# Performance work log

Hardware: AMD Instinct MI355X
Metric: run time of the kernel (lower is better)

The kernel has to match this reference:

```python
import jax, jax.numpy as jnp
import numpy as np

B = 16384          # batch (parallel envs)
D_OBS = 512        # num_actor_obs
A = 32             # num_actions
E = 8              # num_experts
K = 2              # top_k
GH = [256, 128]    # gating hidden dims
EH = [1024, 512, 256]  # expert hidden dims


def _linear_init(key, fan_in, fan_out, extra=()):
    kw, kb = jax.random.split(key)
    scale = 1.0 / np.sqrt(fan_in)
    w = jax.random.uniform(kw, extra + (fan_in, fan_out), jnp.float32, -scale, scale)
    b = jax.random.uniform(kb, extra + (fan_out,), jnp.float32, -scale, scale)
    return w, b


def setup_inputs() -> dict:
    key = jax.random.key(0)
    ks = jax.random.split(key, 8)
    obs = jax.random.normal(ks[0], (B, D_OBS), jnp.float32)
    # gating network: D_OBS -> 256 -> 128 -> E
    gw1, gb1 = _linear_init(ks[1], D_OBS, GH[0])
    gw2, gb2 = _linear_init(ks[2], GH[0], GH[1])
    gw3, gb3 = _linear_init(ks[3], GH[1], E)
    # experts (stacked over expert axis): D_OBS -> 1024 -> 512 -> 256 -> A
    ew1, eb1 = _linear_init(ks[4], D_OBS, EH[0], (E,))
    ew2, eb2 = _linear_init(ks[5], EH[0], EH[1], (E,))
    ew3, eb3 = _linear_init(ks[6], EH[1], EH[2], (E,))
    ew4, eb4 = _linear_init(ks[7], EH[2], A, (E,))
    return {
        "observations": obs,
        "gw1": gw1, "gb1": gb1, "gw2": gw2, "gb2": gb2, "gw3": gw3, "gb3": gb3,
        "ew1": ew1, "eb1": eb1, "ew2": ew2, "eb2": eb2,
        "ew3": ew3, "eb3": eb3, "ew4": ew4, "eb4": eb4,
    }


def reference(observations, gw1, gb1, gw2, gb2, gw3, gb3,
              ew1, eb1, ew2, eb2, ew3, eb3, ew4, eb4):
    elu = jax.nn.elu
    # --- gating network ---
    g = elu(observations @ gw1 + gb1)
    g = elu(g @ gw2 + gb2)
    gate_logits = g @ gw3 + gb3                      # [B, E]
    gate_probs = jax.nn.softmax(gate_logits, axis=-1)
    # --- top-k selection and renormalization ---
    topk_w, topk_idx = jax.lax.top_k(gate_probs, K)  # [B, K]
    topk_w = topk_w / jnp.sum(topk_w, axis=-1, keepdims=True)
    # --- run all experts as batched GEMMs (same math as masked dispatch) ---
    h = elu(jnp.einsum('bi,eio->beo', observations, ew1) + eb1)  # [B, E, 1024]
    h = elu(jnp.einsum('beo,eoh->beh', h, ew2) + eb2)            # [B, E, 512]
    h = elu(jnp.einsum('beh,ehf->bef', h, ew3) + eb3)            # [B, E, 256]
    expert_out = jnp.einsum('bef,efa->bea', h, ew4) + eb4        # [B, E, A]
    # --- weighted combine over selected experts ---
    onehot = jax.nn.one_hot(topk_idx, E, dtype=topk_w.dtype)     # [B, K, E]
    combine_w = jnp.einsum('bk,bke->be', topk_w, onehot)         # [B, E]
    action_mean = jnp.einsum('be,bea->ba', combine_w, expert_out)  # [B, A]
    return action_mean
```

## Files before the change

### kernel.cpp

```cpp
#include <hip/hip_runtime.h>
#include <hip/hip_bf16.h>

typedef __bf16 v8bf __attribute__((ext_vector_type(8)));
typedef float  v4f  __attribute__((ext_vector_type(4)));

#define B_ROWS 16384
#define NSLOTS 32768
#define MAXTILES 264

#define OFF_W1T   0u
#define OFF_W2T   8388608u
#define OFF_W3T   16777216u
#define OFF_W4T   18874368u
#define OFF_META  19005440u
#define OFF_SEL   19009536u
#define OFF_W01   19075072u
#define OFF_ROWL  19206144u
#define OFF_WL    19337216u
#define OFF_Q     19468288u
#define OFF_G1    OFF_Q
#define OFF_G2    (OFF_Q + 16777216u)
#define OFF_X1    OFF_Q
#define OFF_H2    OFF_Q
#define OFF_EO    OFF_Q
#define OFF_H1    (OFF_Q + 33554432u)
#define OFF_H3    OFF_H1
#define WS_NEED   (OFF_H1 + 67108864u)


__device__ __forceinline__ void gload_lds16(const void* g, void* l) {
  __builtin_amdgcn_global_load_lds(
      (const __attribute__((address_space(1))) void*)g,
      (__attribute__((address_space(3))) void*)l, 16, 0, 0);
}

__device__ __forceinline__ float elu_f(float x) {
  return x > 0.f ? x : expm1f(x);
}

__global__ __launch_bounds__(256) void transpose_convert(
    const float* __restrict__ in, __hip_bfloat16* __restrict__ outp, int R, int C) {
  __shared__ __align__(16) float tile[32][33];
  int e = blockIdx.z;
  const float* src = in + (size_t)e * R * C;
  __hip_bfloat16* dst = outp + (size_t)e * R * C;
  int r0 = blockIdx.x * 32, c0 = blockIdx.y * 32;
  int tr = threadIdx.x >> 5, tc = threadIdx.x & 31;
#pragma unroll
  for (int q = 0; q < 4; ++q)
    tile[tr + 8*q][tc] = src[(size_t)(r0 + tr + 8*q) * C + c0 + tc];
  __syncthreads();
#pragma unroll
  for (int q = 0; q < 4; ++q)
    dst[(size_t)(c0 + tr + 8*q) * R + r0 + tc] = __float2bfloat16(tile[tc][tr + 8*q]);
}

__global__ __launch_bounds__(256) void sgemm_elu(
    const float* __restrict__ A, const float* __restrict__ Bm,
    const float* __restrict__ bias, float* __restrict__ C,
    int M, int N, int K) {
  __shared__ __align__(16) float sA[16][132];
  __shared__ __align__(16) float sB[16][68];
  int tid = threadIdx.x;
  int tx = tid & 15, ty = tid >> 4;
  int m0 = blockIdx.x * 128, n0 = blockIdx.y * 64;
  float acc[8][4] = {};
  for (int k0 = 0; k0 < K; k0 += 16) {
    {
      int m = tid >> 1, ks = (tid & 1) * 8;
      const float* ap = &A[(size_t)(m0 + m) * K + k0 + ks];
      float4 v0 = *(const float4*)ap;
      float4 v1 = *(const float4*)(ap + 4);
      sA[ks+0][m] = v0.x; sA[ks+1][m] = v0.y; sA[ks+2][m] = v0.z; sA[ks+3][m] = v0.w;
      sA[ks+4][m] = v1.x; sA[ks+5][m] = v1.y; sA[ks+6][m] = v1.z; sA[ks+7][m] = v1.w;
    }
    {
      int kr = tid >> 4, nn = (tid & 15) * 4;
      *(float4*)&sB[kr][nn] = *(const float4*)&Bm[(size_t)(k0 + kr) * N + n0 + nn];
    }
    __syncthreads();
#pragma unroll
    for (int kk = 0; kk < 16; ++kk) {
      float a[8], b[4];
      *(float4*)&a[0] = *(const float4*)&sA[kk][ty*8];
      *(float4*)&a[4] = *(const float4*)&sA[kk][ty*8+4];
      *(float4*)&b[0] = *(const float4*)&sB[kk][tx*4];
#pragma unroll
      for (int i = 0; i < 8; ++i)
#pragma unroll
        for (int j = 0; j < 4; ++j)
          acc[i][j] = fmaf(a[i], b[j], acc[i][j]);
    }
    __syncthreads();
  }
  float bs[4];
#pragma unroll
  for (int j = 0; j < 4; ++j) bs[j] = bias[n0 + tx*4 + j];
#pragma unroll
  for (int i = 0; i < 8; ++i) {
    int m = m0 + ty*8 + i;
    float4 o;
    o.x = elu_f(acc[i][0] + bs[0]);
    o.y = elu_f(acc[i][1] + bs[1]);
    o.z = elu_f(acc[i][2] + bs[2]);
    o.w = elu_f(acc[i][3] + bs[3]);
    *(float4*)&C[(size_t)m * N + n0 + tx*4] = o;
  }
}

__global__ __launch_bounds__(256) void gate3_topk(
    const float* __restrict__ G2, const float* __restrict__ gw3,
    const float* __restrict__ gb3, int* __restrict__ sel01,
    float2* __restrict__ w01, int* __restrict__ meta) {
  __shared__ __align__(16) float g2t[64][132];
  __shared__ __align__(16) float w3[1024];
  __shared__ float b3[8];
  __shared__ int lc[8];
  int tid = threadIdx.x;
  int row0 = blockIdx.x * 64;
  {
    int r = tid >> 5, f = (tid & 31) * 4;
#pragma unroll
    for (int rr = 0; rr < 64; rr += 8)
      *(float4*)&g2t[r + rr][f] = *(const float4*)&G2[(size_t)(row0 + r + rr) * 128 + f];
  }
  ((float4*)w3)[tid] = ((const float4*)gw3)[tid];
  if (tid < 8) { b3[tid] = gb3[tid]; lc[tid] = 0; }
  __syncthreads();
  if (tid < 64) {
    int row = row0 + tid;
    float lg[8];
#pragma unroll
    for (int e = 0; e < 8; ++e) lg[e] = b3[e];
    for (int k = 0; k < 128; ++k) {
      float x = g2t[tid][k];
#pragma unroll
      for (int e = 0; e < 8; ++e) lg[e] = fmaf(x, w3[k*8 + e], lg[e]);
    }
    float mx = lg[0];
#pragma unroll
    for (int e = 1; e < 8; ++e) mx = fmaxf(mx, lg[e]);
    float p[8], s = 0.f;
#pragma unroll
    for (int e = 0; e < 8; ++e) { p[e] = expf(lg[e] - mx); s += p[e]; }
    float inv = 1.f / s;
#pragma unroll
    for (int e = 0; e < 8; ++e) p[e] *= inv;
    int i0 = 0; float v0 = p[0];
#pragma unroll
    for (int e = 1; e < 8; ++e) if (p[e] > v0) { v0 = p[e]; i0 = e; }
    int i1 = -1; float v1 = -1.f;
#pragma unroll
    for (int e = 0; e < 8; ++e) if (e != i0 && p[e] > v1) { v1 = p[e]; i1 = e; }
    float sw = 1.f / (v0 + v1);
    sel01[row] = i0 | (i1 << 8);
    w01[row] = make_float2(v0 * sw, v1 * sw);
    atomicAdd(&lc[i0], 1);
    atomicAdd(&lc[i1], 1);
  }
  __syncthreads();
  if (tid < 8) atomicAdd(&meta[1 + tid], lc[tid]);
}

__global__ void build_tiles(int* __restrict__ meta) {
  if (threadIdx.x != 0) return;
  int base = 0, nt = 0;
  for (int e = 0; e < 8; ++e) {
    int c = meta[1 + e];
    meta[17 + e] = base;
    for (int j = 0; j < c; j += 128) {
      meta[32 + nt]  = e;
      meta[296 + nt] = base + j;
      meta[560 + nt] = (c - j < 128) ? (c - j) : 128;
      nt++;
    }
    base += c;
  }
  meta[0] = nt;
}

__global__ __launch_bounds__(256) void scatter_rows(
    const int* __restrict__ sel01, float2* __restrict__ w01,
    int* __restrict__ meta, int* __restrict__ rowlist, float* __restrict__ wlist) {
  __shared__ int lc[8];
  __shared__ int gb[8];
  int tid = threadIdx.x;
  if (tid < 8) lc[tid] = 0;
  __syncthreads();
  int row = blockIdx.x * 256 + tid;
  int s = sel01[row];
  int e0 = s & 255, e1 = (s >> 8) & 255;
  float2 w = w01[row];
  int l0 = atomicAdd(&lc[e0], 1);
  int l1 = atomicAdd(&lc[e1], 1);
  __syncthreads();
  if (tid < 8) gb[tid] = atomicAdd(&meta[9 + tid], lc[tid]);
  __syncthreads();
  int s0 = meta[17 + e0] + gb[e0] + l0;
  int s1 = meta[17 + e1] + gb[e1] + l1;
  rowlist[s0] = row; wlist[s0] = w.x;
  rowlist[s1] = row; wlist[s1] = w.y;
  ((int2*)w01)[row] = make_int2(s0, s1);
}

__global__ __launch_bounds__(256) void gather_convert(
    const float* __restrict__ obs, const int* __restrict__ rowlist,
    __hip_bfloat16* __restrict__ X1) {
  int tid = threadIdx.x;
  int slot = blockIdx.x * 4 + (tid >> 6);
  int l = tid & 63;
  int row = rowlist[slot];
  const float* src = obs + (size_t)row * 512 + l * 8;
  float4 a = *(const float4*)src;
  float4 b = *(const float4*)(src + 4);
  union { __hip_bfloat16 h[8]; uint4 u; } t;
  t.h[0] = __float2bfloat16(a.x); t.h[1] = __float2bfloat16(a.y);
  t.h[2] = __float2bfloat16(a.z); t.h[3] = __float2bfloat16(a.w);
  t.h[4] = __float2bfloat16(b.x); t.h[5] = __float2bfloat16(b.y);
  t.h[6] = __float2bfloat16(b.z); t.h[7] = __float2bfloat16(b.w);
  *(uint4*)(X1 + (size_t)slot * 512 + l * 8) = t.u;
}

__global__ __launch_bounds__(256) void moe_gemm(
    const __hip_bfloat16* __restrict__ A, const __hip_bfloat16* __restrict__ BT,
    const float* __restrict__ bias, __hip_bfloat16* __restrict__ C,
    const int* __restrict__ meta, int N, int K) {
  int t = blockIdx.x;
  if (t >= meta[0]) return;
  int e    = meta[32 + t];
  int m0   = meta[296 + t];
  int rows = meta[560 + t];
  int n0   = blockIdx.y * 128;

  __shared__ __align__(16) __hip_bfloat16 sA[128 * 32];
  __shared__ __align__(16) __hip_bfloat16 sB[128 * 32];

  int tid = threadIdx.x;
  int w = tid >> 6, l = tid & 63;
  int lr = l >> 2;
  int lk = (l & 3) * 8;
  int wm = w >> 1, wn = w & 1;
  int ml = l & 15, kq = l >> 4;

  const __hip_bfloat16* BTe = BT + (size_t)e * N * K;
  v4f acc[4][4] = {};

  for (int k0 = 0; k0 < K; k0 += 32) {
#pragma unroll
    for (int it = 0; it < 2; ++it) {
      int r = it * 64 + w * 16 + lr;
      int gr = m0 + (r < rows ? r : rows - 1);
      gload_lds16(A + (size_t)gr * K + k0 + lk, &sA[(it * 64 + w * 16) * 32]);
    }
#pragma unroll
    for (int it = 0; it < 2; ++it) {
      int r = it * 64 + w * 16 + lr;
      gload_lds16(BTe + (size_t)(n0 + r) * K + k0 + lk, &sB[(it * 64 + w * 16) * 32]);
    }
    __syncthreads();
    v8bf af[4], bf[4];
#pragma unroll
    for (int i = 0; i < 4; ++i)
      af[i] = *(const v8bf*)&sA[(wm * 64 + i * 16 + ml) * 32 + kq * 8];
#pragma unroll
    for (int j = 0; j < 4; ++j)
      bf[j] = *(const v8bf*)&sB[(wn * 64 + j * 16 + ml) * 32 + kq * 8];
#pragma unroll
    for (int i = 0; i < 4; ++i)
#pragma unroll
      for (int j = 0; j < 4; ++j)
        acc[i][j] = __builtin_amdgcn_mfma_f32_16x16x32_bf16(af[i], bf[j], acc[i][j], 0, 0, 0);
    __syncthreads();
  }

  int rl0 = kq * 4;
#pragma unroll
  for (int j = 0; j < 4; ++j) {
    int col = n0 + wn * 64 + j * 16 + ml;
    float bs = bias[(size_t)e * N + col];
#pragma unroll
    for (int i = 0; i < 4; ++i) {
#pragma unroll
      for (int r = 0; r < 4; ++r) {
        int rl = wm * 64 + i * 16 + rl0 + r;
        if (rl < rows) {
          float v = elu_f(acc[i][j][r] + bs);
          C[(size_t)(m0 + rl) * N + col] = __float2bfloat16(v);
        }
      }
    }
  }
}

__global__ __launch_bounds__(256) void l4_gemm(
    const __hip_bfloat16* __restrict__ H3, const __hip_bfloat16* __restrict__ W4T,
    const float* __restrict__ eb4, const int* __restrict__ meta,
    float* __restrict__ EO) {
  int t = blockIdx.x;
  if (t >= meta[0]) return;
  int e = meta[32 + t], m0 = meta[296 + t], rows = meta[560 + t];
  __shared__ __align__(16) __hip_bfloat16 sW[32 * 264];
  int tid = threadIdx.x;
  {
    const uint4* src = (const uint4*)(W4T + (size_t)e * 8192);
#pragma unroll
    for (int q = 0; q < 4; ++q) {
      int c = tid + 256 * q;
      int r = c >> 5, col = (c & 31) * 8;
      *(uint4*)&sW[r * 264 + col] = src[c];
    }
  }
  __syncthreads();
  int w = tid >> 6, l = tid & 63;
  int ml = l & 15, kq = l >> 4;
  v4f acc[2][2] = {};
  const __hip_bfloat16* Abase = H3 + (size_t)m0 * 256;
#pragma unroll
  for (int k0 = 0; k0 < 256; k0 += 32) {
    v8bf af[2], bf[2];
#pragma unroll
    for (int i = 0; i < 2; ++i) {
      int r = w * 32 + i * 16 + ml;
      int rr = r < rows ? r : 0;
      af[i] = *(const v8bf*)(Abase + (size_t)rr * 256 + k0 + kq * 8);
    }
#pragma unroll
    for (int j = 0; j < 2; ++j)
      bf[j] = *(const v8bf*)&sW[(j * 16 + ml) * 264 + k0 + kq * 8];
#pragma unroll
    for (int i = 0; i < 2; ++i)
#pragma unroll
      for (int j = 0; j < 2; ++j)
        acc[i][j] = __builtin_amdgcn_mfma_f32_16x16x32_bf16(af[i], bf[j], acc[i][j], 0, 0, 0);
  }
#pragma unroll
  for (int j = 0; j < 2; ++j) {
    int col = j * 16 + ml;
    float bs = eb4[e * 32 + col];
#pragma unroll
    for (int i = 0; i < 2; ++i) {
#pragma unroll
      for (int r = 0; r < 4; ++r) {
        int rl = w * 32 + i * 16 + kq * 4 + r;
        if (rl < rows)
          EO[(size_t)(m0 + rl) * 32 + col] = acc[i][j][r] + bs;
      }
    }
  }
}

__global__ __launch_bounds__(256) void combine_out(
    const float* __restrict__ EO, const int2* __restrict__ invmap,
    const float* __restrict__ wlist, float* __restrict__ out) {
  int gid = blockIdx.x * 256 + threadIdx.x;
  int row = gid >> 3, q = (gid & 7) * 4;
  int2 s = invmap[row];
  float w0 = wlist[s.x], w1 = wlist[s.y];
  float4 a = *(const float4*)(EO + (size_t)s.x * 32 + q);
  float4 b = *(const float4*)(EO + (size_t)s.y * 32 + q);
  float4 o;
  o.x = w0 * a.x + w1 * b.x;
  o.y = w0 * a.y + w1 * b.y;
  o.z = w0 * a.z + w1 * b.z;
  o.w = w0 * a.w + w1 * b.w;
  *(float4*)(out + (size_t)row * 32 + q) = o;
}

extern "C" void kernel_launch(void* const* d_in, const int* in_sizes, int n_in,
                              void* d_out, int out_size, void* d_ws, size_t ws_size,
                              hipStream_t stream) {
  const float* obs = (const float*)d_in[0];
  const float* gw1 = (const float*)d_in[1];
  const float* gb1 = (const float*)d_in[2];
  const float* gw2 = (const float*)d_in[3];
  const float* gb2 = (const float*)d_in[4];
  const float* gw3 = (const float*)d_in[5];
  const float* gb3 = (const float*)d_in[6];
  const float* ew1 = (const float*)d_in[7];
  const float* eb1 = (const float*)d_in[8];
  const float* ew2 = (const float*)d_in[9];
  const float* eb2 = (const float*)d_in[10];
  const float* ew3 = (const float*)d_in[11];
  const float* eb3 = (const float*)d_in[12];
  const float* ew4 = (const float*)d_in[13];
  const float* eb4 = (const float*)d_in[14];

  if (ws_size < (size_t)WS_NEED) return;

  char* ws = (char*)d_ws;
  __hip_bfloat16* W1T = (__hip_bfloat16*)(ws + OFF_W1T);
  __hip_bfloat16* W2T = (__hip_bfloat16*)(ws + OFF_W2T);
  __hip_bfloat16* W3T = (__hip_bfloat16*)(ws + OFF_W3T);
  __hip_bfloat16* W4T = (__hip_bfloat16*)(ws + OFF_W4T);
  int*    meta    = (int*)(ws + OFF_META);
  int*    sel01   = (int*)(ws + OFF_SEL);
  float2* w01     = (float2*)(ws + OFF_W01);
  int*    rowlist = (int*)(ws + OFF_ROWL);
  float*  wlist   = (float*)(ws + OFF_WL);
  float*  G1      = (float*)(ws + OFF_G1);
  float*  G2      = (float*)(ws + OFF_G2);
  __hip_bfloat16* X1 = (__hip_bfloat16*)(ws + OFF_X1);
  __hip_bfloat16* H1 = (__hip_bfloat16*)(ws + OFF_H1);
  __hip_bfloat16* H2 = (__hip_bfloat16*)(ws + OFF_H2);
  __hip_bfloat16* H3 = (__hip_bfloat16*)(ws + OFF_H3);
  float* EO       = (float*)(ws + OFF_EO);
  float* outp = (float*)d_out;

  (void)hipMemsetAsync(meta, 0, 128, stream);

  transpose_convert<<<dim3(16, 32, 8), 256, 0, stream>>>(ew1, W1T, 512, 1024);
  transpose_convert<<<dim3(32, 16, 8), 256, 0, stream>>>(ew2, W2T, 1024, 512);
  transpose_convert<<<dim3(16,  8, 8), 256, 0, stream>>>(ew3, W3T, 512, 256);
  transpose_convert<<<dim3( 8,  1, 8), 256, 0, stream>>>(ew4, W4T, 256, 32);

  sgemm_elu<<<dim3(128, 4), 256, 0, stream>>>(obs, gw1, gb1, G1, B_ROWS, 256, 512);
  sgemm_elu<<<dim3(128, 2), 256, 0, stream>>>(G1, gw2, gb2, G2, B_ROWS, 128, 256);
  gate3_topk<<<256, 256, 0, stream>>>(G2, gw3, gb3, sel01, w01, meta);
  build_tiles<<<1, 64, 0, stream>>>(meta);
  scatter_rows<<<64, 256, 0, stream>>>(sel01, w01, meta, rowlist, wlist);
  gather_convert<<<8192, 256, 0, stream>>>(obs, rowlist, X1);

  moe_gemm<<<dim3(MAXTILES, 8), 256, 0, stream>>>(X1, W1T, eb1, H1, meta, 1024, 512);
  moe_gemm<<<dim3(MAXTILES, 4), 256, 0, stream>>>(H1, W2T, eb2, H2, meta, 512, 1024);
  moe_gemm<<<dim3(MAXTILES, 2), 256, 0, stream>>>(H2, W3T, eb3, H3, meta, 256, 512);
  l4_gemm<<<MAXTILES, 256, 0, stream>>>(H3, W4T, eb4, meta, EO);
  combine_out<<<512, 256, 0, stream>>>(EO, (const int2*)w01, wlist, outp);
}
```

Before: 490.4 us.

## Stage MoE GEMM epilogue through LDS, swizzle tile order, merge weight transposes

```diff
diff --git a/kernel.cpp b/kernel.cpp
--- a/kernel.cpp
+++ b/kernel.cpp
@@ -3,10 +3,12 @@
 
 typedef __bf16 v8bf __attribute__((ext_vector_type(8)));
 typedef float  v4f  __attribute__((ext_vector_type(4)));
+typedef unsigned int v4u __attribute__((ext_vector_type(4)));
 
 #define B_ROWS 16384
 #define NSLOTS 32768
 #define MAXTILES 264
+#define CSTRIDE 136
 
 #define OFF_W1T   0u
 #define OFF_W2T   8388608u
@@ -27,6 +29,13 @@
 #define OFF_H3    OFF_H1
 #define WS_NEED   (OFF_H1 + 67108864u)
 
+#undef  OFF_H2
+#undef  OFF_EO
+#define OFF_H2B   (OFF_H1 + 67108864u)
+#define OFF_EO2   OFF_Q
+#undef  WS_NEED
+#define WS_NEED   (OFF_H2B + 33554432u)
+
 
 __device__ __forceinline__ void gload_lds16(const void* g, void* l) {
   __builtin_amdgcn_global_load_lds(
@@ -38,13 +47,22 @@
   return x > 0.f ? x : expm1f(x);
 }
 
-__global__ __launch_bounds__(256) void transpose_convert(
-    const float* __restrict__ in, __hip_bfloat16* __restrict__ outp, int R, int C) {
+__global__ __launch_bounds__(256) void transpose_all(
+    const float* __restrict__ ew1, const float* __restrict__ ew2,
+    const float* __restrict__ ew3, const float* __restrict__ ew4,
+    __hip_bfloat16* __restrict__ W1T, __hip_bfloat16* __restrict__ W2T,
+    __hip_bfloat16* __restrict__ W3T, __hip_bfloat16* __restrict__ W4T) {
   __shared__ __align__(16) float tile[32][33];
-  int e = blockIdx.z;
-  const float* src = in + (size_t)e * R * C;
-  __hip_bfloat16* dst = outp + (size_t)e * R * C;
-  int r0 = blockIdx.x * 32, c0 = blockIdx.y * 32;
+  int b = blockIdx.x;
+  const float* src; __hip_bfloat16* dst; int R, C, gxs, tps, idx;
+  if (b < 4096)      { src = ew1; dst = W1T; R = 512;  C = 1024; gxs = 4; tps = 9; idx = b; }
+  else if (b < 8192) { src = ew2; dst = W2T; R = 1024; C = 512;  gxs = 5; tps = 9; idx = b - 4096; }
+  else if (b < 9216) { src = ew3; dst = W3T; R = 512;  C = 256;  gxs = 4; tps = 7; idx = b - 8192; }
+  else               { src = ew4; dst = W4T; R = 256;  C = 32;   gxs = 3; tps = 3; idx = b - 9216; }
+  int e = idx >> tps, tt = idx & ((1 << tps) - 1);
+  int r0 = (tt & ((1 << gxs) - 1)) * 32, c0 = (tt >> gxs) * 32;
+  src += (size_t)e * R * C;
+  dst += (size_t)e * R * C;
   int tr = threadIdx.x >> 5, tc = threadIdx.x & 31;
 #pragma unroll
   for (int q = 0; q < 4; ++q)
@@ -213,27 +231,33 @@
   const float* src = obs + (size_t)row * 512 + l * 8;
   float4 a = *(const float4*)src;
   float4 b = *(const float4*)(src + 4);
-  union { __hip_bfloat16 h[8]; uint4 u; } t;
+  union { __hip_bfloat16 h[8]; v4u u; } t;
   t.h[0] = __float2bfloat16(a.x); t.h[1] = __float2bfloat16(a.y);
   t.h[2] = __float2bfloat16(a.z); t.h[3] = __float2bfloat16(a.w);
   t.h[4] = __float2bfloat16(b.x); t.h[5] = __float2bfloat16(b.y);
   t.h[6] = __float2bfloat16(b.z); t.h[7] = __float2bfloat16(b.w);
-  *(uint4*)(X1 + (size_t)slot * 512 + l * 8) = t.u;
+  *(v4u*)(X1 + (size_t)slot * 512 + l * 8) = t.u;
 }
 
 __global__ __launch_bounds__(256) void moe_gemm(
     const __hip_bfloat16* __restrict__ A, const __hip_bfloat16* __restrict__ BT,
     const float* __restrict__ bias, __hip_bfloat16* __restrict__ C,
-    const int* __restrict__ meta, int N, int K) {
-  int t = blockIdx.x;
+    const int* __restrict__ meta, int N, int K, int lgNB) {
+  int b = blockIdx.x;
+  int c = b & 7;
+  int j = (b >> 3) & ((1 << lgNB) - 1);
+  int m = b >> (3 + lgNB);
+  int t = m * 8 + c;
   if (t >= meta[0]) return;
   int e    = meta[32 + t];
   int m0   = meta[296 + t];
   int rows = meta[560 + t];
-  int n0   = blockIdx.y * 128;
-
-  __shared__ __align__(16) __hip_bfloat16 sA[128 * 32];
-  __shared__ __align__(16) __hip_bfloat16 sB[128 * 32];
+  int n0   = j * 128;
+
+  __shared__ __align__(16) char smem[CSTRIDE * 64 * 2 > 16384 ? CSTRIDE * 64 * 2 : 16384];
+  __hip_bfloat16* sA  = (__hip_bfloat16*)smem;
+  __hip_bfloat16* sB  = (__hip_bfloat16*)(smem + 8192);
+  __hip_bfloat16* cst = (__hip_bfloat16*)smem;
 
   int tid = threadIdx.x;
   int w = tid >> 6, l = tid & 63;
@@ -263,32 +287,46 @@
     for (int i = 0; i < 4; ++i)
       af[i] = *(const v8bf*)&sA[(wm * 64 + i * 16 + ml) * 32 + kq * 8];
 #pragma unroll
-    for (int j = 0; j < 4; ++j)
-      bf[j] = *(const v8bf*)&sB[(wn * 64 + j * 16 + ml) * 32 + kq * 8];
+    for (int jj = 0; jj < 4; ++jj)
+      bf[jj] = *(const v8bf*)&sB[(wn * 64 + jj * 16 + ml) * 32 + kq * 8];
 #pragma unroll
     for (int i = 0; i < 4; ++i)
 #pragma unroll
-      for (int j = 0; j < 4; ++j)
-        acc[i][j] = __builtin_amdgcn_mfma_f32_16x16x32_bf16(af[i], bf[j], acc[i][j], 0, 0, 0);
-    __syncthreads();
-  }
-
-  int rl0 = kq * 4;
-#pragma unroll
-  for (int j = 0; j < 4; ++j) {
-    int col = n0 + wn * 64 + j * 16 + ml;
-    float bs = bias[(size_t)e * N + col];
-#pragma unroll
-    for (int i = 0; i < 4; ++i) {
-#pragma unroll
-      for (int r = 0; r < 4; ++r) {
-        int rl = wm * 64 + i * 16 + rl0 + r;
-        if (rl < rows) {
-          float v = elu_f(acc[i][j][r] + bs);
-          C[(size_t)(m0 + rl) * N + col] = __float2bfloat16(v);
-        }
+      for (int jj = 0; jj < 4; ++jj)
+        acc[i][jj] = __builtin_amdgcn_mfma_f32_16x16x32_bf16(af[i], bf[jj], acc[i][jj], 0, 0, 0);
+    __syncthreads();
+  }
+
+  float bs[4];
+#pragma unroll
+  for (int jj = 0; jj < 4; ++jj)
+    bs[jj] = bias[(size_t)e * N + n0 + wn * 64 + jj * 16 + ml];
+
+#pragma unroll
+  for (int h = 0; h < 2; ++h) {
+    if (wm == h) {
+#pragma unroll
+      for (int i = 0; i < 4; ++i)
+#pragma unroll
+        for (int jj = 0; jj < 4; ++jj)
+#pragma unroll
+          for (int r = 0; r < 4; ++r)
+            cst[(i * 16 + kq * 4 + r) * CSTRIDE + wn * 64 + jj * 16 + ml] =
+                __float2bfloat16(elu_f(acc[i][jj][r] + bs[jj]));
+    }
+    __syncthreads();
+#pragma unroll
+    for (int q = 0; q < 4; ++q) {
+      int z = q * 256 + tid;
+      int row = z >> 4, ch = z & 15;
+      int rl = h * 64 + row;
+      if (rl < rows) {
+        v4u v = *(const v4u*)&cst[row * CSTRIDE + ch * 8];
+        __builtin_nontemporal_store(
+            v, (v4u*)&C[(size_t)(m0 + rl) * N + n0 + ch * 8]);
       }
     }
+    __syncthreads();
   }
 }
 
@@ -401,17 +439,14 @@
   float*  G2      = (float*)(ws + OFF_G2);
   __hip_bfloat16* X1 = (__hip_bfloat16*)(ws + OFF_X1);
   __hip_bfloat16* H1 = (__hip_bfloat16*)(ws + OFF_H1);
-  __hip_bfloat16* H2 = (__hip_bfloat16*)(ws + OFF_H2);
+  __hip_bfloat16* H2 = (__hip_bfloat16*)(ws + OFF_H2B);
   __hip_bfloat16* H3 = (__hip_bfloat16*)(ws + OFF_H3);
-  float* EO       = (float*)(ws + OFF_EO);
+  float* EO       = (float*)(ws + OFF_EO2);
   float* outp = (float*)d_out;
 
   (void)hipMemsetAsync(meta, 0, 128, stream);
 
-  transpose_convert<<<dim3(16, 32, 8), 256, 0, stream>>>(ew1, W1T, 512, 1024);
-  transpose_convert<<<dim3(32, 16, 8), 256, 0, stream>>>(ew2, W2T, 1024, 512);
-  transpose_convert<<<dim3(16,  8, 8), 256, 0, stream>>>(ew3, W3T, 512, 256);
-  transpose_convert<<<dim3( 8,  1, 8), 256, 0, stream>>>(ew4, W4T, 256, 32);
+  transpose_all<<<9280, 256, 0, stream>>>(ew1, ew2, ew3, ew4, W1T, W2T, W3T, W4T);
 
   sgemm_elu<<<dim3(128, 4), 256, 0, stream>>>(obs, gw1, gb1, G1, B_ROWS, 256, 512);
   sgemm_elu<<<dim3(128, 2), 256, 0, stream>>>(G1, gw2, gb2, G2, B_ROWS, 128, 256);
@@ -420,9 +455,9 @@
   scatter_rows<<<64, 256, 0, stream>>>(sel01, w01, meta, rowlist, wlist);
   gather_convert<<<8192, 256, 0, stream>>>(obs, rowlist, X1);
 
-  moe_gemm<<<dim3(MAXTILES, 8), 256, 0, stream>>>(X1, W1T, eb1, H1, meta, 1024, 512);
-  moe_gemm<<<dim3(MAXTILES, 4), 256, 0, stream>>>(H1, W2T, eb2, H2, meta, 512, 1024);
-  moe_gemm<<<dim3(MAXTILES, 2), 256, 0, stream>>>(H2, W3T, eb3, H3, meta, 256, 512);
+  moe_gemm<<<MAXTILES * 8, 256, 0, stream>>>(X1, W1T, eb1, H1, meta, 1024, 512, 3);
+  moe_gemm<<<MAXTILES * 4, 256, 0, stream>>>(H1, W2T, eb2, H2, meta, 512, 1024, 2);
+  moe_gemm<<<MAXTILES * 2, 256, 0, stream>>>(H2, W3T, eb3, H3, meta, 256, 512, 1);
   l4_gemm<<<MAXTILES, 256, 0, stream>>>(H3, W4T, eb4, meta, EO);
   combine_out<<<512, 256, 0, stream>>>(EO, (const int2*)w01, wlist, outp);
 }
```

After: 481.4 us. No clear change (-1.8%).
